# Kernel tuning notes

Measured on AMD Instinct MI355X. Metric: run time of the kernel, lower is better.

## Reference

```python
import jax, jax.numpy as jnp
import numpy as np

D = 1024      # n_embd
H = 16        # n_head
HD = D // H   # head_size = 64


def _layernorm(x, g, b, eps=1e-5):
    mu = jnp.mean(x, axis=-1, keepdims=True)
    var = jnp.mean((x - mu) ** 2, axis=-1, keepdims=True)
    return (x - mu) * jax.lax.rsqrt(var + eps) * g + b


def setup_inputs() -> dict:
    key = jax.random.key(0)
    ks = jax.random.split(key, 12)
    s = lambda fan_in: 1.0 / np.sqrt(fan_in)
    inp = {
        "x": jax.random.normal(ks[0], (4, 2048, D), dtype=jnp.float32),
        # attention projections (bias=False in Head), per-head weights fused into [D, D]
        "wq": jax.random.uniform(ks[1], (D, D), jnp.float32, -s(D), s(D)),
        "wk": jax.random.uniform(ks[2], (D, D), jnp.float32, -s(D), s(D)),
        "wv": jax.random.uniform(ks[3], (D, D), jnp.float32, -s(D), s(D)),
        "wo": jax.random.uniform(ks[4], (D, D), jnp.float32, -s(D), s(D)),
        "bo": jax.random.uniform(ks[5], (D,), jnp.float32, -s(D), s(D)),
        # feed-forward: D -> 4D -> D
        "w1": jax.random.uniform(ks[6], (D, 4 * D), jnp.float32, -s(D), s(D)),
        "b1": jax.random.uniform(ks[7], (4 * D,), jnp.float32, -s(D), s(D)),
        "w2": jax.random.uniform(ks[8], (4 * D, D), jnp.float32, -s(4 * D), s(4 * D)),
        "b2": jax.random.uniform(ks[9], (D,), jnp.float32, -s(4 * D), s(4 * D)),
        # layernorms
        "g_ln1": jnp.ones((D,), jnp.float32),
        "b_ln1": jnp.zeros((D,), jnp.float32),
        "g_ln2": jnp.ones((D,), jnp.float32),
        "b_ln2": jnp.zeros((D,), jnp.float32),
    }
    return inp


def reference(x, wq, wk, wv, wo, bo, w1, b1, w2, b2, g_ln1, b_ln1, g_ln2, b_ln2):
    B, T, _ = x.shape
    # --- self-attention on ln1(x) ---
    h = _layernorm(x, g_ln1, b_ln1)
    q = (h @ wq).reshape(B, T, H, HD)
    k = (h @ wk).reshape(B, T, H, HD)
    v = (h @ wv).reshape(B, T, H, HD)
    scores = jnp.einsum("bqhd,bkhd->bhqk", q, k) * (HD ** -0.5)
    causal = jnp.tril(jnp.ones((T, T), dtype=bool))
    scores = jnp.where(causal, scores, -jnp.inf)
    wei = jax.nn.softmax(scores, axis=-1)                    # [B,H,T,T]
    attn = jnp.einsum("bhqk,bkhd->bqhd", wei, v).reshape(B, T, D)
    x = x + attn @ wo + bo
    # --- feed-forward on ln2(x) ---
    h2 = _layernorm(x, g_ln2, b_ln2)
    x = x + jax.nn.relu(h2 @ w1 + b1) @ w2 + b2
    return x
```

## Files before the change

kernel.cpp:

```cpp
#include <hip/hip_runtime.h>
#include <cstdint>

typedef __bf16 bf16x8 __attribute__((ext_vector_type(8)));
typedef float f32x4 __attribute__((ext_vector_type(4)));
typedef unsigned int u32x4 __attribute__((ext_vector_type(4)));
typedef unsigned short u16x4 __attribute__((ext_vector_type(4)));

#define D_MODEL 1024
#define SEQ     2048
#define NBATCH  4
#define NHEAD   16
#define HDIM    64
#define NTOK    (NBATCH * SEQ)
#define QSCALE  0.18033688011112042f

__device__ __forceinline__ unsigned short f2bf(float f) {
  unsigned int u = __builtin_bit_cast(unsigned int, f);
  u += 0x7FFFu + ((u >> 16) & 1u);
  return (unsigned short)(u >> 16);
}

__device__ __forceinline__ bf16x8 load8bf(const unsigned short* p) {
  return __builtin_bit_cast(bf16x8, *(const u32x4*)p);
}

__device__ __forceinline__ f32x4 mfma16(bf16x8 a, bf16x8 b, f32x4 c) {
  return __builtin_amdgcn_mfma_f32_16x16x32_bf16(a, b, c, 0, 0, 0);
}

__device__ __forceinline__ void gload16(const unsigned short* g, unsigned short* l) {
  __builtin_amdgcn_global_load_lds((__attribute__((address_space(1))) void*)g,
                                   (__attribute__((address_space(3))) void*)l, 16, 0, 0);
}

__global__ __launch_bounds__(256) void tcast_all(const float* __restrict__ wq,
                                                 const float* __restrict__ wk,
                                                 const float* __restrict__ wv,
                                                 const float* __restrict__ wo,
                                                 const float* __restrict__ w1,
                                                 const float* __restrict__ w2,
                                                 unsigned short* __restrict__ wqkv_t,
                                                 unsigned short* __restrict__ wo_t,
                                                 unsigned short* __restrict__ w1_t,
                                                 unsigned short* __restrict__ w2_t) {
  const int id = blockIdx.x;
  const float* in; unsigned short* out; int K, N, k0, n0;
  if (id < 4096) {
    const int seg = id >> 10, r = id & 1023;
    in  = seg == 0 ? wq : seg == 1 ? wk : seg == 2 ? wv : wo;
    out = seg == 3 ? wo_t : wqkv_t + (size_t)seg * 1024 * 1024;
    K = 1024; N = 1024; n0 = (r & 31) * 32; k0 = (r >> 5) * 32;
  } else if (id < 8192) {
    const int r = id - 4096;
    in = w1; out = w1_t; K = 1024; N = 4096;
    n0 = (r & 127) * 32; k0 = (r >> 7) * 32;
  } else {
    const int r = id - 8192;
    in = w2; out = w2_t; K = 4096; N = 1024;
    n0 = (r & 31) * 32; k0 = (r >> 5) * 32;
  }
  __shared__ float tile[32][33];
  const int tx = threadIdx.x & 31, ty = threadIdx.x >> 5;
  #pragma unroll
  for (int j = 0; j < 4; ++j)
    tile[ty + 8 * j][tx] = in[(size_t)(k0 + ty + 8 * j) * N + n0 + tx];
  __syncthreads();
  #pragma unroll
  for (int j = 0; j < 4; ++j)
    out[(size_t)(n0 + ty + 8 * j) * K + k0 + tx] = f2bf(tile[tx][ty + 8 * j]);
}

__global__ __launch_bounds__(256) void ln_kernel(const float* __restrict__ x,
                                                 const float* __restrict__ g,
                                                 const float* __restrict__ bb,
                                                 unsigned short* __restrict__ out) {
  const int row = blockIdx.x, tid = threadIdx.x;
  const float4 xv = ((const float4*)(x + (size_t)row * D_MODEL))[tid];
  float s  = xv.x + xv.y + xv.z + xv.w;
  float ss = xv.x * xv.x + xv.y * xv.y + xv.z * xv.z + xv.w * xv.w;
  #pragma unroll
  for (int off = 1; off < 64; off <<= 1) { s += __shfl_xor(s, off); ss += __shfl_xor(ss, off); }
  __shared__ float red[8];
  const int wave = tid >> 6, lane = tid & 63;
  if (lane == 0) { red[wave] = s; red[4 + wave] = ss; }
  __syncthreads();
  s  = red[0] + red[1] + red[2] + red[3];
  ss = red[4] + red[5] + red[6] + red[7];
  const float mu   = s * (1.0f / D_MODEL);
  const float var  = ss * (1.0f / D_MODEL) - mu * mu;
  const float rstd = rsqrtf(var + 1e-5f);
  const float4 gv = ((const float4*)g)[tid];
  const float4 bv = ((const float4*)bb)[tid];
  u16x4 o;
  o.x = f2bf((xv.x - mu) * rstd * gv.x + bv.x);
  o.y = f2bf((xv.y - mu) * rstd * gv.y + bv.y);
  o.z = f2bf((xv.z - mu) * rstd * gv.z + bv.z);
  o.w = f2bf((xv.w - mu) * rstd * gv.w + bv.w);
  *(u16x4*)(out + (size_t)row * D_MODEL + tid * 4) = o;
}

template <bool BIAS, bool RELU, bool RES, bool OBF, bool QKV>
__global__ __launch_bounds__(256) void gemm_bt(const unsigned short* __restrict__ A,
                                               const unsigned short* __restrict__ Bt,
                                               const float* __restrict__ bias,
                                               const float* __restrict__ res,
                                               void* __restrict__ out,
                                               unsigned short* __restrict__ qb,
                                               unsigned short* __restrict__ kp,
                                               unsigned short* __restrict__ vt,
                                               int M, int N, int K) {
  __shared__ __align__(16) unsigned short As[128 * 64];
  __shared__ __align__(16) unsigned short Bs[128 * 64];
  const int tid  = threadIdx.x;
  const int lin = blockIdx.y * gridDim.x + blockIdx.x;
  const int xcd = lin & 7, idx = lin >> 3;
  const int by = xcd * 8 + (idx & 7);
  const int bx = idx >> 3;
  const int row0 = by * 128, col0 = bx * 128;
  const int wave = tid >> 6, lane = tid & 63;
  const int wm = wave >> 1, wn = wave & 1;
  const int l15 = lane & 15, quad = lane >> 4;
  f32x4 acc[4][4] = {};

  const int tr = tid >> 3;
  const int tc = (tid & 7) ^ (tr & 7);
  const unsigned short* gA = A  + (size_t)(row0 + tr) * K + tc * 8;
  const unsigned short* gB = Bt + (size_t)(col0 + tr) * K + tc * 8;

  const int rowA = (wm * 64 + l15) * 64;
  const int rowB = (wn * 64 + l15) * 64;
  const int swz0 = (quad ^ (l15 & 7)) * 8;
  const int swz1 = ((4 + quad) ^ (l15 & 7)) * 8;

  for (int k0 = 0; k0 < K; k0 += 64) {
    #pragma unroll
    for (int i = 0; i < 4; ++i) {
      gload16(gA + (size_t)(i * 32) * K + k0, As + (i * 256 + tid) * 8);
      gload16(gB + (size_t)(i * 32) * K + k0, Bs + (i * 256 + tid) * 8);
    }
    __syncthreads();
    #pragma unroll
    for (int kf = 0; kf < 2; ++kf) {
      const int swz = kf ? swz1 : swz0;
      bf16x8 af[4], bfr[4];
      #pragma unroll
      for (int t = 0; t < 4; ++t) {
        af[t]  = load8bf(As + rowA + t * 1024 + swz);
        bfr[t] = load8bf(Bs + rowB + t * 1024 + swz);
      }
      #pragma unroll
      for (int i = 0; i < 4; ++i)
        #pragma unroll
        for (int j = 0; j < 4; ++j)
          acc[i][j] = mfma16(af[i], bfr[j], acc[i][j]);
    }
    __syncthreads();
  }

  const size_t rbase = (size_t)row0 + wm * 64 + quad * 4;
  const int cbase = col0 + wn * 64 + l15;
  if (QKV) {
    const int sec = col0 >> 10;
    #pragma unroll
    for (int i = 0; i < 4; ++i) {
      #pragma unroll
      for (int j = 0; j < 4; ++j) {
        const int col = cbase + j * 16;
        if (sec == 0) {
          #pragma unroll
          for (int r = 0; r < 4; ++r) {
            const size_t row = rbase + i * 16 + r;
            qb[row * 1024 + col] = f2bf(acc[i][j][r] * QSCALE);
          }
        } else if (sec == 1) {
          const int c2 = col - 1024, hh = c2 >> 6, d = c2 & 63;
          #pragma unroll
          for (int r = 0; r < 4; ++r) {
            const size_t row = rbase + i * 16 + r;
            const int bb = (int)(row >> 11), t = (int)(row & 2047);
            kp[(((size_t)(bb * 16 + hh)) * SEQ + t) * 64 + d] = f2bf(acc[i][j][r]);
          }
        } else {
          const int c2 = col - 2048, hh = c2 >> 6, d = c2 & 63;
          const size_t t0 = rbase + i * 16;
          const int bb = (int)(t0 >> 11);
          u16x4 pk;
          #pragma unroll
          for (int r = 0; r < 4; ++r) pk[r] = f2bf(acc[i][j][r]);
          *(u16x4*)(vt + ((size_t)(bb * 16 + hh) * 64 + d) * SEQ + (t0 & 2047)) = pk;
        }
      }
    }
  } else {
    #pragma unroll
    for (int i = 0; i < 4; ++i) {
      #pragma unroll
      for (int j = 0; j < 4; ++j) {
        const int col = cbase + j * 16;
        const float bval = BIAS ? bias[col] : 0.0f;
        #pragma unroll
        for (int r = 0; r < 4; ++r) {
          const size_t row = rbase + i * 16 + r;
          float v = acc[i][j][r];
          if (BIAS) v += bval;
          if (RELU) v = fmaxf(v, 0.0f);
          if (RES)  v += res[row * N + col];
          if (OBF)  ((unsigned short*)out)[row * N + col] = f2bf(v);
          else      ((float*)out)[row * N + col] = v;
        }
      }
    }
  }
}

__global__ __launch_bounds__(256) void attn4(const unsigned short* __restrict__ qb,
                                             const unsigned short* __restrict__ kp,
                                             const unsigned short* __restrict__ vt,
                                             unsigned short* __restrict__ attnb) {
  const int lin = (blockIdx.z * 16 + blockIdx.y) * 8 + blockIdx.x;
  const int xcd = lin & 7, idx = lin >> 3;
  const int bh = xcd * 8 + (idx >> 3);
  const int xb = idx & 7;
  const int b = bh >> 4, h = bh & 15;
  const int tid = threadIdx.x, wave = tid >> 6, lane = tid & 63;
  const int l15 = lane & 15, quad = lane >> 4;
  const size_t tokbase = (size_t)b * SEQ;

  __shared__ __align__(16) unsigned short ks[64 * 64];
  __shared__ __align__(16) unsigned short vts[64 * 64];
  __shared__ __align__(16) unsigned short plds[4][32 * 64];

  const unsigned short* kbase = kp + (size_t)bh * SEQ * HDIM;
  const unsigned short* vbase = vt + (size_t)bh * HDIM * SEQ;

  for (int half = 0; half < 2; ++half) {
    const int qblk = (half == 0) ? (15 - xb) : xb;
    const int qw0 = qblk * 128 + wave * 32;

    bf16x8 qf[2][2];
    #pragma unroll
    for (int mf = 0; mf < 2; ++mf)
      #pragma unroll
      for (int kf = 0; kf < 2; ++kf)
        qf[mf][kf] = load8bf(qb + (tokbase + qw0 + mf * 16 + l15) * 1024
                             + h * HDIM + kf * 32 + quad * 8);

    f32x4 o[2][4] = {};
    float lsum[2][4] = {};

    const int ntiles = qblk * 2 + 2;
    for (int kt = 0; kt < ntiles; ++kt) {
      const int k0 = kt * 64;
      __syncthreads();
      #pragma unroll
      for (int i = 0; i < 2; ++i) {
        const int cid = i * 256 + tid;
        const int r = cid >> 3, p = cid & 7, c = p ^ (r & 7);
        gload16(kbase + (size_t)(k0 + r) * HDIM + c * 8, ks + cid * 8);
      }
      #pragma unroll
      for (int i = 0; i < 2; ++i) {
        const int cid = i * 256 + tid;
        const int d = cid >> 3, p = cid & 7, c = p ^ (d & 7);
        gload16(vbase + (size_t)d * SEQ + k0 + c * 8, vts + cid * 8);
      }
      __syncthreads();
      if (k0 <= qw0 + 31) {
        f32x4 s[2][4] = {};
        #pragma unroll
        for (int kf = 0; kf < 2; ++kf)
          #pragma unroll
          for (int nf = 0; nf < 4; ++nf) {
            const int row = nf * 16 + l15;
            const int p = (kf * 4 + quad) ^ (row & 7);
            const bf16x8 bk = load8bf(ks + row * 64 + p * 8);
            s[0][nf] = mfma16(qf[0][kf], bk, s[0][nf]);
            s[1][nf] = mfma16(qf[1][kf], bk, s[1][nf]);
          }
        #pragma unroll
        for (int mf = 0; mf < 2; ++mf)
          #pragma unroll
          for (int nf = 0; nf < 4; ++nf) {
            const int key = k0 + nf * 16 + l15;
            #pragma unroll
            for (int r = 0; r < 4; ++r) {
              const int lq = mf * 16 + quad * 4 + r;
              float p = __builtin_amdgcn_exp2f(s[mf][nf][r]);
              p = (key > qw0 + lq) ? 0.0f : p;
              const unsigned int pu = __builtin_bit_cast(unsigned int, p);
              lsum[mf][r] += __builtin_bit_cast(float, pu & 0xFFFF0000u);
              const int pc = ((nf * 16 + l15) >> 3) ^ (lq & 7) ^ ((lq >> 3) & 3);
              plds[wave][lq * 64 + pc * 8 + (l15 & 7)] = (unsigned short)(pu >> 16);
            }
          }
        __builtin_amdgcn_s_waitcnt(0);
        #pragma unroll
        for (int kf = 0; kf < 2; ++kf) {
          bf16x8 pa[2];
          #pragma unroll
          for (int mf = 0; mf < 2; ++mf) {
            const int lq = mf * 16 + l15;
            const int p = (kf * 4 + quad) ^ (lq & 7) ^ ((lq >> 3) & 3);
            pa[mf] = load8bf(&plds[wave][lq * 64 + p * 8]);
          }
          #pragma unroll
          for (int df = 0; df < 4; ++df) {
            const int row = df * 16 + l15;
            const int p = (kf * 4 + quad) ^ (row & 7);
            const bf16x8 vb = load8bf(vts + row * 64 + p * 8);
            o[0][df] = mfma16(pa[0], vb, o[0][df]);
            o[1][df] = mfma16(pa[1], vb, o[1][df]);
          }
        }
      }
    }
    #pragma unroll
    for (int mf = 0; mf < 2; ++mf)
      #pragma unroll
      for (int r = 0; r < 4; ++r) {
        float l = lsum[mf][r];
        #pragma unroll
        for (int off = 1; off < 16; off <<= 1) l += __shfl_xor(l, off);
        const float rl = 1.0f / l;
        const size_t row = tokbase + qw0 + mf * 16 + quad * 4 + r;
        #pragma unroll
        for (int df = 0; df < 4; ++df)
          attnb[row * D_MODEL + h * HDIM + df * 16 + l15] = f2bf(o[mf][df][r] * rl);
      }
  }
}

extern "C" void kernel_launch(void* const* d_in, const int* in_sizes, int n_in,
                              void* d_out, int out_size, void* d_ws, size_t ws_size,
                              hipStream_t stream) {
  const float* x    = (const float*)d_in[0];
  const float* wq   = (const float*)d_in[1];
  const float* wk   = (const float*)d_in[2];
  const float* wv   = (const float*)d_in[3];
  const float* wo   = (const float*)d_in[4];
  const float* bo   = (const float*)d_in[5];
  const float* w1   = (const float*)d_in[6];
  const float* b1   = (const float*)d_in[7];
  const float* w2   = (const float*)d_in[8];
  const float* b2   = (const float*)d_in[9];
  const float* g1   = (const float*)d_in[10];
  const float* bl1  = (const float*)d_in[11];
  const float* g2   = (const float*)d_in[12];
  const float* bl2  = (const float*)d_in[13];
  float* out = (float*)d_out;

  char* ws = (char*)d_ws;
  size_t off = 0;
  auto alloc = [&](size_t bytes) { char* p = ws + off; off += (bytes + 255) & ~(size_t)255; return p; };
  unsigned short* wqkv_t = (unsigned short*)alloc((size_t)3072 * 1024 * 2);
  unsigned short* wo_t   = (unsigned short*)alloc((size_t)1024 * 1024 * 2);
  unsigned short* w1_t   = (unsigned short*)alloc((size_t)4096 * 1024 * 2);
  unsigned short* w2_t   = (unsigned short*)alloc((size_t)1024 * 4096 * 2);
  unsigned short* h1     = (unsigned short*)alloc((size_t)NTOK * 1024 * 2);
  unsigned short* kpb    = (unsigned short*)alloc((size_t)NTOK * 1024 * 2);
  unsigned short* vtb    = (unsigned short*)alloc((size_t)NTOK * 1024 * 2);
  unsigned short* attnb  = (unsigned short*)alloc((size_t)NTOK * 1024 * 2);
  unsigned short* h2     = (unsigned short*)alloc((size_t)NTOK * 1024 * 2);
  unsigned short* ffn1   = (unsigned short*)alloc((size_t)NTOK * 4096 * 2);
  unsigned short* qb = attnb;

  tcast_all<<<12288, 256, 0, stream>>>(wq, wk, wv, wo, w1, w2,
                                       wqkv_t, wo_t, w1_t, w2_t);
  ln_kernel<<<NTOK, 256, 0, stream>>>(x, g1, bl1, h1);
  gemm_bt<false, false, false, true, true><<<dim3(24, 64), 256, 0, stream>>>(
      h1, wqkv_t, nullptr, nullptr, nullptr, qb, kpb, vtb, NTOK, 3072, 1024);
  attn4<<<dim3(SEQ / 256, NHEAD, NBATCH), 256, 0, stream>>>(qb, kpb, vtb, attnb);
  gemm_bt<true, false, true, false, false><<<dim3(8, 64), 256, 0, stream>>>(
      attnb, wo_t, bo, x, out, nullptr, nullptr, nullptr, NTOK, 1024, 1024);
  ln_kernel<<<NTOK, 256, 0, stream>>>(out, g2, bl2, h2);
  gemm_bt<true, true, false, true, false><<<dim3(32, 64), 256, 0, stream>>>(
      h2, w1_t, b1, nullptr, ffn1, nullptr, nullptr, nullptr, NTOK, 4096, 1024);
  gemm_bt<true, false, true, false, false><<<dim3(8, 64), 256, 0, stream>>>(
      ffn1, w2_t, b2, out, out, nullptr, nullptr, nullptr, NTOK, 1024, 4096);
  (void)in_sizes; (void)n_in; (void)out_size; (void)ws_size;
}
```

Baseline: 479.4 us.

## Transpose attention score MFMA and store residual stream in bf16

The attention kernel now computes S^T (keys as the A operand), so each lane holds four consecutive keys for one query. That lets P be packed into 8-byte LDS writes with a simpler swizzle, and the row sum reduces to two shuffles instead of four per row. The intermediate residual x1 is also written as bf16 into a reused buffer. The second layernorm and the final GEMM's residual add read bf16 instead of fp32, which cuts memory traffic but lowers residual precision.

```diff
diff --git a/kernel.cpp b/kernel.cpp
--- a/kernel.cpp
+++ b/kernel.cpp
@@ -4,6 +4,7 @@
 typedef __bf16 bf16x8 __attribute__((ext_vector_type(8)));
 typedef float f32x4 __attribute__((ext_vector_type(4)));
 typedef unsigned int u32x4 __attribute__((ext_vector_type(4)));
+typedef unsigned int u32x2 __attribute__((ext_vector_type(2)));
 typedef unsigned short u16x4 __attribute__((ext_vector_type(4)));
 
 #define D_MODEL 1024
@@ -18,6 +19,10 @@
   unsigned int u = __builtin_bit_cast(unsigned int, f);
   u += 0x7FFFu + ((u >> 16) & 1u);
   return (unsigned short)(u >> 16);
+}
+
+__device__ __forceinline__ float bf2f(unsigned short s) {
+  return __builtin_bit_cast(float, (unsigned int)s << 16);
 }
 
 __device__ __forceinline__ bf16x8 load8bf(const unsigned short* p) {
@@ -70,12 +75,19 @@
     out[(size_t)(n0 + ty + 8 * j) * K + k0 + tx] = f2bf(tile[tx][ty + 8 * j]);
 }
 
-__global__ __launch_bounds__(256) void ln_kernel(const float* __restrict__ x,
+template <int FPIN>
+__global__ __launch_bounds__(256) void ln_kernel(const void* __restrict__ xin,
                                                  const float* __restrict__ g,
                                                  const float* __restrict__ bb,
                                                  unsigned short* __restrict__ out) {
   const int row = blockIdx.x, tid = threadIdx.x;
-  const float4 xv = ((const float4*)(x + (size_t)row * D_MODEL))[tid];
+  float4 xv;
+  if (FPIN) {
+    xv = ((const float4*)((const float*)xin + (size_t)row * D_MODEL))[tid];
+  } else {
+    const u16x4 bv4 = ((const u16x4*)((const unsigned short*)xin + (size_t)row * D_MODEL))[tid];
+    xv.x = bf2f(bv4.x); xv.y = bf2f(bv4.y); xv.z = bf2f(bv4.z); xv.w = bf2f(bv4.w);
+  }
   float s  = xv.x + xv.y + xv.z + xv.w;
   float ss = xv.x * xv.x + xv.y * xv.y + xv.z * xv.z + xv.w * xv.w;
   #pragma unroll
@@ -99,11 +111,11 @@
   *(u16x4*)(out + (size_t)row * D_MODEL + tid * 4) = o;
 }
 
-template <bool BIAS, bool RELU, bool RES, bool OBF, bool QKV>
+template <bool BIAS, bool RELU, int RES, bool OBF, bool QKV>
 __global__ __launch_bounds__(256) void gemm_bt(const unsigned short* __restrict__ A,
                                                const unsigned short* __restrict__ Bt,
                                                const float* __restrict__ bias,
-                                               const float* __restrict__ res,
+                                               const void* __restrict__ res,
                                                void* __restrict__ out,
                                                unsigned short* __restrict__ qb,
                                                unsigned short* __restrict__ kp,
@@ -204,7 +216,8 @@
           float v = acc[i][j][r];
           if (BIAS) v += bval;
           if (RELU) v = fmaxf(v, 0.0f);
-          if (RES)  v += res[row * N + col];
+          if (RES == 1) v += ((const float*)res)[row * N + col];
+          if (RES == 2) v += bf2f(((const unsigned short*)res)[row * N + col]);
           if (OBF)  ((unsigned short*)out)[row * N + col] = f2bf(v);
           else      ((float*)out)[row * N + col] = v;
         }
@@ -213,7 +226,7 @@
   }
 }
 
-__global__ __launch_bounds__(256) void attn4(const unsigned short* __restrict__ qb,
+__global__ __launch_bounds__(256) void attn5(const unsigned short* __restrict__ qb,
                                              const unsigned short* __restrict__ kp,
                                              const unsigned short* __restrict__ vt,
                                              unsigned short* __restrict__ attnb) {
@@ -239,14 +252,14 @@
 
     bf16x8 qf[2][2];
     #pragma unroll
-    for (int mf = 0; mf < 2; ++mf)
+    for (int qfi = 0; qfi < 2; ++qfi)
       #pragma unroll
       for (int kf = 0; kf < 2; ++kf)
-        qf[mf][kf] = load8bf(qb + (tokbase + qw0 + mf * 16 + l15) * 1024
-                             + h * HDIM + kf * 32 + quad * 8);
+        qf[qfi][kf] = load8bf(qb + (tokbase + qw0 + qfi * 16 + l15) * 1024
+                              + h * HDIM + kf * 32 + quad * 8);
 
     f32x4 o[2][4] = {};
-    float lsum[2][4] = {};
+    float lsum[2] = {0.0f, 0.0f};
 
     const int ntiles = qblk * 2 + 2;
     for (int kt = 0; kt < ntiles; ++kt) {
@@ -266,33 +279,39 @@
       }
       __syncthreads();
       if (k0 <= qw0 + 31) {
-        f32x4 s[2][4] = {};
+        f32x4 s[4][2] = {};
         #pragma unroll
         for (int kf = 0; kf < 2; ++kf)
           #pragma unroll
-          for (int nf = 0; nf < 4; ++nf) {
-            const int row = nf * 16 + l15;
+          for (int keyf = 0; keyf < 4; ++keyf) {
+            const int row = keyf * 16 + l15;
             const int p = (kf * 4 + quad) ^ (row & 7);
-            const bf16x8 bk = load8bf(ks + row * 64 + p * 8);
-            s[0][nf] = mfma16(qf[0][kf], bk, s[0][nf]);
-            s[1][nf] = mfma16(qf[1][kf], bk, s[1][nf]);
-          }
-        #pragma unroll
-        for (int mf = 0; mf < 2; ++mf)
-          #pragma unroll
-          for (int nf = 0; nf < 4; ++nf) {
-            const int key = k0 + nf * 16 + l15;
+            const bf16x8 kfr = load8bf(ks + row * 64 + p * 8);
+            s[keyf][0] = mfma16(kfr, qf[0][kf], s[keyf][0]);
+            s[keyf][1] = mfma16(kfr, qf[1][kf], s[keyf][1]);
+          }
+        #pragma unroll
+        for (int qfi = 0; qfi < 2; ++qfi) {
+          const int q = qw0 + qfi * 16 + l15;
+          const int qloc = qfi * 16 + l15;
+          #pragma unroll
+          for (int keyf = 0; keyf < 4; ++keyf) {
+            unsigned int pw[4];
             #pragma unroll
             for (int r = 0; r < 4; ++r) {
-              const int lq = mf * 16 + quad * 4 + r;
-              float p = __builtin_amdgcn_exp2f(s[mf][nf][r]);
-              p = (key > qw0 + lq) ? 0.0f : p;
-              const unsigned int pu = __builtin_bit_cast(unsigned int, p);
-              lsum[mf][r] += __builtin_bit_cast(float, pu & 0xFFFF0000u);
-              const int pc = ((nf * 16 + l15) >> 3) ^ (lq & 7) ^ ((lq >> 3) & 3);
-              plds[wave][lq * 64 + pc * 8 + (l15 & 7)] = (unsigned short)(pu >> 16);
+              const int key = k0 + keyf * 16 + quad * 4 + r;
+              float p = __builtin_amdgcn_exp2f(s[keyf][qfi][r]);
+              p = (key > q) ? 0.0f : p;
+              pw[r] = __builtin_bit_cast(unsigned int, p);
+              lsum[qfi] += __builtin_bit_cast(float, pw[r] & 0xFFFF0000u);
             }
-          }
+            u32x2 packed;
+            packed.x = (pw[0] >> 16) | (pw[1] & 0xFFFF0000u);
+            packed.y = (pw[2] >> 16) | (pw[3] & 0xFFFF0000u);
+            const int slot = (keyf * 4 + quad) ^ ((l15 & 7) << 1);
+            *(u32x2*)(&plds[wave][qloc * 64 + slot * 4]) = packed;
+          }
+        }
         __builtin_amdgcn_s_waitcnt(0);
         #pragma unroll
         for (int kf = 0; kf < 2; ++kf) {
@@ -300,8 +319,8 @@
           #pragma unroll
           for (int mf = 0; mf < 2; ++mf) {
             const int lq = mf * 16 + l15;
-            const int p = (kf * 4 + quad) ^ (lq & 7) ^ ((lq >> 3) & 3);
-            pa[mf] = load8bf(&plds[wave][lq * 64 + p * 8]);
+            const int c = (kf * 4 + quad) ^ (l15 & 7);
+            pa[mf] = load8bf(&plds[wave][lq * 64 + c * 8]);
           }
           #pragma unroll
           for (int df = 0; df < 4; ++df) {
@@ -315,18 +334,20 @@
       }
     }
     #pragma unroll
-    for (int mf = 0; mf < 2; ++mf)
+    for (int mf = 0; mf < 2; ++mf) {
+      float l = lsum[mf];
+      l += __shfl_xor(l, 16);
+      l += __shfl_xor(l, 32);
+      const float rl = 1.0f / l;
       #pragma unroll
       for (int r = 0; r < 4; ++r) {
-        float l = lsum[mf][r];
-        #pragma unroll
-        for (int off = 1; off < 16; off <<= 1) l += __shfl_xor(l, off);
-        const float rl = 1.0f / l;
+        const float rv = __shfl(rl, quad * 4 + r);
         const size_t row = tokbase + qw0 + mf * 16 + quad * 4 + r;
         #pragma unroll
         for (int df = 0; df < 4; ++df)
-          attnb[row * D_MODEL + h * HDIM + df * 16 + l15] = f2bf(o[mf][df][r] * rl);
-      }
+          attnb[row * D_MODEL + h * HDIM + df * 16 + l15] = f2bf(o[mf][df][r] * rv);
+      }
+    }
   }
 }
 
@@ -362,20 +383,21 @@
   unsigned short* attnb  = (unsigned short*)alloc((size_t)NTOK * 1024 * 2);
   unsigned short* h2     = (unsigned short*)alloc((size_t)NTOK * 1024 * 2);
   unsigned short* ffn1   = (unsigned short*)alloc((size_t)NTOK * 4096 * 2);
-  unsigned short* qb = attnb;
+  unsigned short* qb  = attnb;
+  unsigned short* x1b = h1;
 
   tcast_all<<<12288, 256, 0, stream>>>(wq, wk, wv, wo, w1, w2,
                                        wqkv_t, wo_t, w1_t, w2_t);
-  ln_kernel<<<NTOK, 256, 0, stream>>>(x, g1, bl1, h1);
-  gemm_bt<false, false, false, true, true><<<dim3(24, 64), 256, 0, stream>>>(
+  ln_kernel<1><<<NTOK, 256, 0, stream>>>(x, g1, bl1, h1);
+  gemm_bt<false, false, 0, true, true><<<dim3(24, 64), 256, 0, stream>>>(
       h1, wqkv_t, nullptr, nullptr, nullptr, qb, kpb, vtb, NTOK, 3072, 1024);
-  attn4<<<dim3(SEQ / 256, NHEAD, NBATCH), 256, 0, stream>>>(qb, kpb, vtb, attnb);
-  gemm_bt<true, false, true, false, false><<<dim3(8, 64), 256, 0, stream>>>(
-      attnb, wo_t, bo, x, out, nullptr, nullptr, nullptr, NTOK, 1024, 1024);
-  ln_kernel<<<NTOK, 256, 0, stream>>>(out, g2, bl2, h2);
-  gemm_bt<true, true, false, true, false><<<dim3(32, 64), 256, 0, stream>>>(
+  attn5<<<dim3(SEQ / 256, NHEAD, NBATCH), 256, 0, stream>>>(qb, kpb, vtb, attnb);
+  gemm_bt<true, false, 1, true, false><<<dim3(8, 64), 256, 0, stream>>>(
+      attnb, wo_t, bo, x, x1b, nullptr, nullptr, nullptr, NTOK, 1024, 1024);
+  ln_kernel<0><<<NTOK, 256, 0, stream>>>(x1b, g2, bl2, h2);
+  gemm_bt<true, true, 0, true, false><<<dim3(32, 64), 256, 0, stream>>>(
       h2, w1_t, b1, nullptr, ffn1, nullptr, nullptr, nullptr, NTOK, 4096, 1024);
-  gemm_bt<true, false, true, false, false><<<dim3(8, 64), 256, 0, stream>>>(
-      ffn1, w2_t, b2, out, out, nullptr, nullptr, nullptr, NTOK, 1024, 4096);
+  gemm_bt<true, false, 2, false, false><<<dim3(8, 64), 256, 0, stream>>>(
+      ffn1, w2_t, b2, x1b, out, nullptr, nullptr, nullptr, NTOK, 1024, 4096);
   (void)in_sizes; (void)n_in; (void)out_size; (void)ws_size;
 }
```

New measurement: 467.3 us. 2.5% less time.
